# Performance work log

Measured on AMD Instinct MI355X. Metric: run time of the kernel, lower is better.

Reference implementation:

```python
import jax, jax.numpy as jnp
import numpy as np

B, H_IMG, W_IMG, K = 4, 60, 80, 8
HW = H_IMG * W_IMG
IMG_D, PT_D = 192, 128
NH, DH = 6, 64
INNER = NH * DH
NHF = 6
POS_D = 2 * (2 * NHF + 1)  # harmonic emb of 2-d offset, append_input=True -> 26
MAX_DIST = 0.1


def setup_inputs() -> dict:
    key = jax.random.key(0)
    ks = jax.random.split(key, 6)
    ys, xs = jnp.meshgrid(jnp.linspace(0.0, 1.0, H_IMG), jnp.linspace(0.0, 1.0, W_IMG), indexing='ij')
    img_uv = jnp.stack([xs.reshape(-1), ys.reshape(-1)], axis=-1)  # [HW, 2], normalized pixel grid
    return {
        'feat_2d': jax.random.normal(ks[0], (B, HW, IMG_D), jnp.float32),
        'feat_3d': jax.random.normal(ks[1], (B, HW, PT_D), jnp.float32),
        'proj_uv': jax.random.uniform(ks[2], (B, HW, 2), dtype=jnp.float32),
        'img_uv': img_uv,
        'ln_gamma': jnp.ones((IMG_D,), jnp.float32),
        'q_gamma': jnp.ones((NH, DH), jnp.float32),
        'k_gamma': jnp.ones((NH, DH), jnp.float32),
        'Wq': jax.random.normal(ks[3], (IMG_D, INNER), jnp.float32) * IMG_D ** -0.5,
        'Wkv': jax.random.normal(ks[4], (PT_D + POS_D, 2 * INNER), jnp.float32) * (PT_D + POS_D) ** -0.5,
        'Wout': jax.random.normal(ks[5], (INNER, INNER), jnp.float32) * INNER ** -0.5,
    }


def _layernorm(x, g, eps=1e-5):
    mu = jnp.mean(x, -1, keepdims=True)
    var = jnp.mean((x - mu) ** 2, -1, keepdims=True)
    return (x - mu) * jax.lax.rsqrt(var + eps) * g


def _rmsnorm(x, g):
    # lucidrains-style query/key RMSNorm: l2-normalize last dim, scale by sqrt(dim) * per-head gamma
    n = jnp.maximum(jnp.linalg.norm(x, axis=-1, keepdims=True), 1e-12)
    return x / n * (DH ** 0.5) * g


def reference(feat_2d, feat_3d, proj_uv, img_uv, ln_gamma, q_gamma, k_gamma, Wq, Wkv, Wout):
    # --- kNN: for each image pixel, k nearest projected points (brute force) ---
    d2 = (jnp.sum(img_uv ** 2, -1)[None, :, None]
          + jnp.sum(proj_uv ** 2, -1)[:, None, :]
          - 2.0 * jnp.einsum('qd,bnd->bqn', img_uv, proj_uv))  # [B, HW, HW]
    idx = jax.lax.top_k(-d2, K)[1]  # [B, HW, K] int32 indices

    # --- gather neighbor uv coords and 3d features ---
    knn_uv = img_uv[idx]                                        # [B, HW, K, 2]
    knn_f3 = jnp.take_along_axis(feat_3d, idx.reshape(B, HW * K, 1), axis=1).reshape(B, HW, K, PT_D)
    offset = knn_uv - img_uv[None, :, None, :]                  # [B, HW, K, 2]
    mask = jnp.sum(offset ** 2, -1) <= MAX_DIST ** 2            # [B, HW, K]

    # --- harmonic positional embedding of offsets ---
    freqs = 2.0 ** jnp.arange(NHF, dtype=jnp.float32)
    e = (offset[..., None] * freqs).reshape(B, HW, K, 2 * NHF)
    pos = jnp.concatenate([jnp.sin(e), jnp.cos(e), offset], -1)  # [B, HW, K, 26]

    # --- Q / K / V projections ---
    q = (_layernorm(feat_2d, ln_gamma) @ Wq).reshape(B, HW, NH, DH)
    kv = jnp.concatenate([knn_f3, pos], -1) @ Wkv               # [B, HW, K, 2*INNER]
    k_, v_ = jnp.split(kv, 2, axis=-1)
    k_ = k_.reshape(B, HW, K, NH, DH)
    v_ = v_.reshape(B, HW, K, NH, DH)
    q = _rmsnorm(q, q_gamma)
    k_ = _rmsnorm(k_, k_gamma)

    # --- tiny per-pixel attention (query len 1, key len K), scale=1.0 ---
    scores = jnp.einsum('bnhd,bnkhd->bnhk', q, k_)              # [B, HW, NH, K]
    scores = jnp.where(mask[:, :, None, :], scores, -1e30)
    attn = jax.nn.softmax(scores, axis=-1)
    out = jnp.einsum('bnhk,bnkhd->bnhd', attn, v_).reshape(B, HW, INNER)
    return out @ Wout  # output_type='1d': [B, HW, INNER]
```

## Files before the change

### kernel.cpp

```cpp
#include <hip/hip_runtime.h>
#include <math.h>

#define B_    4
#define HW_   4800
#define K_    8
#define IMGD  192
#define PTD   128
#define NH_   6
#define DH_   64
#define INNER 384
#define KVIN  154
#define QT    8
#define NJ    64
#define XBS   168
#define AST   392
#define KTQ   6
#define KTK   5
#define KTO   12

typedef _Float16 f16;
typedef __attribute__((ext_vector_type(8))) _Float16 f16x8;
typedef __attribute__((ext_vector_type(4))) float f32x4;

__global__ __launch_bounds__(256) void pack_kernel(
    const float* __restrict__ Wq, const float* __restrict__ Wkv,
    const float* __restrict__ Wout, f16* __restrict__ pw)
{
  const int e = blockIdx.x * 256 + threadIdx.x;
  if (e >= 672 * 512) return;
  const int f = e >> 9, r = e & 511, l = r >> 3, j = r & 7;
  const int lm = l & 15, kin = (l >> 4) * 8 + j;
  float v;
  if (f < 144) {
    const int nt = f / 6, kt = f % 6;
    v = Wq[(size_t)(kt * 32 + kin) * INNER + nt * 16 + lm];
  } else if (f < 264) {
    const int g = f - 144, nt = g / 5, kt = g % 5, k = kt * 32 + kin;
    v = (k < KVIN) ? Wkv[(size_t)k * (2 * INNER) + nt * 16 + lm] : 0.f;
  } else if (f < 384) {
    const int g = f - 264, nt = g / 5, kt = g % 5, k = kt * 32 + kin;
    v = (k < KVIN) ? Wkv[(size_t)k * (2 * INNER) + INNER + nt * 16 + lm] : 0.f;
  } else {
    const int g = f - 384, nt = g / 12, kt = g % 12;
    v = Wout[(size_t)(kt * 32 + kin) * INNER + nt * 16 + lm];
  }
  pw[e] = (f16)v;
}

#define KNN_INIT(d, ind)                                                      \
  _Pragma("unroll") for (int s = 0; s < K_; ++s) { d[s] = 3.4e38f; ind[s] = 0x7fffffff; }

#define KNN_INSERT(dd, n, dist, ind)                                          \
  if (dd < dist[K_ - 1]) {                                                    \
    bool placed = false;                                                      \
    _Pragma("unroll") for (int s = K_ - 1; s >= 1; --s) {                     \
      if (!placed) {                                                          \
        if (dd < dist[s - 1]) { dist[s] = dist[s - 1]; ind[s] = ind[s - 1]; } \
        else                  { dist[s] = dd; ind[s] = n; placed = true; }    \
      }                                                                       \
    }                                                                         \
    if (!placed) { dist[0] = dd; ind[0] = n; }                                \
  }

#define KNN_MERGE(dist, ind, qidx)                                            \
  _Pragma("unroll") for (int r = 0; r < K_; ++r) {                            \
    float hd = dist[0]; int hi = ind[0];                                      \
    float bd = hd; int bi = hi;                                               \
    _Pragma("unroll") for (int m = 1; m < 64; m <<= 1) {                      \
      float od = __shfl_xor(bd, m); int oi = __shfl_xor(bi, m);               \
      if (od < bd || (od == bd && oi < bi)) { bd = od; bi = oi; }             \
    }                                                                         \
    const bool won = (hd == bd && hi == bi);                                  \
    _Pragma("unroll") for (int s = 0; s < K_ - 1; ++s) {                      \
      dist[s] = won ? dist[s + 1] : dist[s];                                  \
      ind[s]  = won ? ind[s + 1]  : ind[s];                                   \
    }                                                                         \
    dist[K_ - 1] = won ? 3.4e38f : dist[K_ - 1];                              \
    ind[K_ - 1]  = won ? 0x7fffffff : ind[K_ - 1];                            \
    if (lane == r) idx_out[((size_t)b * HW_ + (qidx)) * K_ + r] = bi;         \
  }

__global__ __launch_bounds__(256) void knn_kernel(
    const float* __restrict__ proj_uv,
    const float* __restrict__ img_uv,
    int* __restrict__ idx_out)
{
#pragma clang fp contract(off)
  __shared__ float2 s_p[HW_];

  const int tid  = threadIdx.x;
  const int wave = tid >> 6;
  const int lane = tid & 63;
  const int blk  = blockIdx.x;
  const int b    = blk / (HW_ / 8);
  const int qA   = (blk % (HW_ / 8)) * 8 + wave * 2;
  const int qB   = qA + 1;

  const float2* pv = reinterpret_cast<const float2*>(proj_uv + (size_t)b * HW_ * 2);
  for (int i = tid; i < HW_; i += 256) s_p[i] = pv[i];
  __syncthreads();

  const float qxA = img_uv[qA * 2], qyA = img_uv[qA * 2 + 1];
  const float qxB = img_uv[qB * 2], qyB = img_uv[qB * 2 + 1];
  const float sqqA = qxA * qxA + qyA * qyA;
  const float sqqB = qxB * qxB + qyB * qyB;

  float dA[K_], dB[K_];
  int   iA[K_], iB[K_];
  KNN_INIT(dA, iA);
  KNN_INIT(dB, iB);

  for (int n = lane; n < HW_; n += 64) {
    const float2 p = s_p[n];
    const float sqp = p.x * p.x + p.y * p.y;
    const float dotA = fmaf(qyA, p.y, qxA * p.x);
    const float ddA  = (sqqA + sqp) - 2.0f * dotA;
    KNN_INSERT(ddA, n, dA, iA);
    const float dotB = fmaf(qyB, p.y, qxB * p.x);
    const float ddB  = (sqqB + sqp) - 2.0f * dotB;
    KNN_INSERT(ddB, n, dB, iB);
  }

  KNN_MERGE(dA, iA, qA);
  KNN_MERGE(dB, iB, qB);
}

__global__ __launch_bounds__(256, 4) void fused_kernel(
    const float* __restrict__ feat_2d,
    const float* __restrict__ feat_3d,
    const float* __restrict__ img_uv,
    const float* __restrict__ ln_gamma,
    const float* __restrict__ q_gamma,
    const float* __restrict__ k_gamma,
    const f16*   __restrict__ pw,
    const int*   __restrict__ idx_ws,
    float* __restrict__ out)
{
  __shared__ alignas(16) f16   s_X[NJ][XBS];
  __shared__ alignas(16) float s_regA[QT * AST];
  __shared__ float s_scores[NJ][NH_];
  __shared__ float s_attn[QT][NH_][K_];
  __shared__ float s_mask[NJ];
  __shared__ int   s_idx[NJ];
  __shared__ float s_offx[NJ];
  __shared__ float s_offy[NJ];
  __shared__ float s_norm[QT * NH_];

  f16* s_f16 = reinterpret_cast<f16*>(s_regA);

  const int tid = threadIdx.x;
  const int b   = blockIdx.y;
  const int q0  = blockIdx.x * QT;
  const int l   = tid & 63;
  const int w   = tid >> 6;
  const int lm  = l & 15;
  const int lg  = l >> 4;

  const f16* pwq = pw;
  const f16* pwk = pw + 144 * 512;
  const f16* pwv = pw + 264 * 512;
  const f16* pwo = pw + 384 * 512;

  if (tid < NJ) {
    const int j  = tid;
    const int q  = q0 + (j >> 3);
    const int id = idx_ws[((size_t)b * HW_ + q) * K_ + (j & 7)];
    s_idx[j] = id;
    const float ax = img_uv[id * 2], ay = img_uv[id * 2 + 1];
    const float bx = img_uv[q * 2],  by = img_uv[q * 2 + 1];
    s_offx[j] = ax - bx; s_offy[j] = ay - by;
    const double dox = (double)ax - (double)bx;
    const double doy = (double)ay - (double)by;
    s_mask[j] = (dox * dox + doy * doy <= 0.010000000000000002) ? 1.f : 0.f;
  }
  {
    unsigned* z = (unsigned*)(s_f16 + 8 * AST);
    for (int o = tid; o < 4 * AST; o += 256) z[o] = 0u;
  }
  {
    const int r  = ((tid >> 6) << 1) | ((tid >> 5) & 1);
    const int sl = tid & 31;
    const float* row = feat_2d + ((size_t)b * HW_ + q0 + r) * IMGD;
    float x[6]; float sum = 0.f, ssq = 0.f;
#pragma unroll
    for (int i = 0; i < 6; ++i) { x[i] = row[sl + 32 * i]; sum += x[i]; ssq += x[i] * x[i]; }
#pragma unroll
    for (int m = 16; m >= 1; m >>= 1) { sum += __shfl_xor(sum, m); ssq += __shfl_xor(ssq, m); }
    const float mu = sum * (1.f / 192.f);
    float var = ssq * (1.f / 192.f) - mu * mu;
    var = fmaxf(var, 0.f);
    const float rstd = rsqrtf(var + 1e-5f);
#pragma unroll
    for (int i = 0; i < 6; ++i) {
      const int c = sl + 32 * i;
      s_f16[r * AST + c] = (f16)((x[i] - mu) * rstd * ln_gamma[c]);
    }
  }
  __syncthreads();

  const int jX = tid >> 2, tsub = tid & 3;
  float4 xf[8];
  {
    const float4* f4 = reinterpret_cast<const float4*>(
        feat_3d + ((size_t)b * HW_ + s_idx[jX]) * PTD) + tsub * 8;
#pragma unroll
    for (int i = 0; i < 8; ++i) xf[i] = f4[i];
  }
  f32x4 qacc[6];
#pragma unroll
  for (int t = 0; t < 6; ++t) qacc[t] = (f32x4){0.f, 0.f, 0.f, 0.f};
  {
    const f16* ar = s_f16 + lm * AST + lg * 8;
#pragma unroll
    for (int kt = 0; kt < KTQ; ++kt) {
      const f16x8 a = *(const f16x8*)(ar + kt * 32);
#pragma unroll
      for (int t = 0; t < 6; ++t) {
        const int nt = w * 6 + t;
        const f16x8 bf = *(const f16x8*)(pwq + (((nt * 6 + kt) << 6) + l) * 8);
        qacc[t] = __builtin_amdgcn_mfma_f32_16x16x32_f16(a, bf, qacc[t], 0, 0, 0);
      }
    }
  }
  {
    f16* xr = &s_X[jX][tsub * 32];
#pragma unroll
    for (int i = 0; i < 8; ++i) {
      xr[i * 4 + 0] = (f16)xf[i].x; xr[i * 4 + 1] = (f16)xf[i].y;
      xr[i * 4 + 2] = (f16)xf[i].z; xr[i * 4 + 3] = (f16)xf[i].w;
    }
    if (tsub == 0) {
      const float ox = s_offx[jX], oy = s_offy[jX];
      f16* xp = &s_X[jX][PTD];
#pragma unroll
      for (int m = 0; m < 6; ++m) {
        const float fr = (float)(1 << m);
        float sx, cx, sy, cy;
        sincosf(ox * fr, &sx, &cx);
        sincosf(oy * fr, &sy, &cy);
        xp[m] = (f16)sx; xp[6 + m] = (f16)sy;
        xp[12 + m] = (f16)cx; xp[18 + m] = (f16)cy;
      }
      xp[24] = (f16)ox; xp[25] = (f16)oy;
#pragma unroll
      for (int m = 26; m < 32; ++m) xp[m] = (f16)0.f;
    }
  }
  __syncthreads();

  if (lg < 2) {
#pragma unroll
    for (int t = 0; t < 6; ++t) {
#pragma unroll
      for (int reg = 0; reg < 4; ++reg) {
        s_regA[(lg * 4 + reg) * AST + (w * 6 + t) * 16 + lm] = qacc[t][reg];
      }
    }
  }
  __syncthreads();

  if (tid < QT * NH_) {
    const int r = tid / NH_, h = tid % NH_;
    const float* v = s_regA + r * AST + h * DH_;
    float ss = 0.f;
#pragma unroll
    for (int d = 0; d < DH_; ++d) ss += v[d] * v[d];
    s_norm[tid] = fmaxf(sqrtf(ss), 1e-12f);
  }
  __syncthreads();

  {
    const int r  = tid >> 5;
    const int c0 = (tid & 31) * 12;
#pragma unroll
    for (int i = 0; i < 12; ++i) {
      const int c = c0 + i;
      const float n = s_norm[r * NH_ + (c >> 6)];
      s_regA[r * AST + c] *= (8.f / n) * q_gamma[c];
    }
  }
  __syncthreads();

  {
    const f16* xh = &s_X[16 * w + lm][lg * 8];
    f16x8 ax[KTK];
#pragma unroll
    for (int kt = 0; kt < KTK; ++kt) ax[kt] = *(const f16x8*)(xh + kt * 32);
    const int rq = 2 * w + (lg >> 1);
    for (int h = 0; h < NH_; ++h) {
      f32x4 kacc[4];
#pragma unroll
      for (int t = 0; t < 4; ++t) kacc[t] = (f32x4){0.f, 0.f, 0.f, 0.f};
#pragma unroll
      for (int kt = 0; kt < KTK; ++kt) {
#pragma unroll
        for (int t = 0; t < 4; ++t) {
          const int nt = h * 4 + t;
          const f16x8 bf = *(const f16x8*)(pwk + (((nt * 5 + kt) << 6) + l) * 8);
          kacc[t] = __builtin_amdgcn_mfma_f32_16x16x32_f16(ax[kt], bf, kacc[t], 0, 0, 0);
        }
      }
      float ss[4], sc[4];
#pragma unroll
      for (int reg = 0; reg < 4; ++reg) { ss[reg] = 0.f; sc[reg] = 0.f; }
#pragma unroll
      for (int t = 0; t < 4; ++t) {
        const int n = h * DH_ + t * 16 + lm;
        const float qg = s_regA[rq * AST + n] * k_gamma[n];
#pragma unroll
        for (int reg = 0; reg < 4; ++reg) {
          const float v = kacc[t][reg];
          ss[reg] += v * v;
          sc[reg] += v * qg;
        }
      }
#pragma unroll
      for (int m = 1; m < 16; m <<= 1) {
#pragma unroll
        for (int reg = 0; reg < 4; ++reg) {
          ss[reg] += __shfl_xor(ss[reg], m);
          sc[reg] += __shfl_xor(sc[reg], m);
        }
      }
      if (lm == 0) {
#pragma unroll
        for (int reg = 0; reg < 4; ++reg) {
          const float nn = fmaxf(sqrtf(ss[reg]), 1e-12f);
          s_scores[16 * w + (lg << 2) + reg][h] = (8.f / nn) * sc[reg];
        }
      }
    }
  }
  __syncthreads();

  if (tid < QT * NH_) {
    const int r = tid / NH_, h = tid % NH_;
    float s[K_]; float mx = -1e38f;
#pragma unroll
    for (int k = 0; k < K_; ++k) {
      float v = s_scores[r * K_ + k][h];
      if (s_mask[r * K_ + k] == 0.f) v = -1e30f;
      s[k] = v; mx = fmaxf(mx, v);
    }
    float sum = 0.f;
#pragma unroll
    for (int k = 0; k < K_; ++k) { const float pp = expf(s[k] - mx); s[k] = pp; sum += pp; }
    const float inv = 1.f / sum;
#pragma unroll
    for (int k = 0; k < K_; ++k) s_attn[r][h][k] = s[k] * inv;
  }
  __syncthreads();

  {
    unsigned* z = (unsigned*)(s_f16 + 8 * AST);
    for (int o = tid; o < 4 * AST; o += 256) z[o] = 0u;
  }
  {
    const int k0 = (lg & 1) * 4;
#pragma unroll
    for (int mt = 0; mt < 4; ++mt) {
      const f16* xh = &s_X[16 * mt + lm][lg * 8];
      f16x8 av[KTK];
#pragma unroll
      for (int kt = 0; kt < KTK; ++kt) av[kt] = *(const f16x8*)(xh + kt * 32);
      const int qrow = 2 * mt + (lg >> 1);
#pragma unroll
      for (int t = 0; t < 6; ++t) {
        const int nt = w * 6 + t;
        const int h  = nt >> 2;
        f32x4 c = (f32x4){0.f, 0.f, 0.f, 0.f};
#pragma unroll
        for (int kt = 0; kt < KTK; ++kt) {
          const f16x8 bf = *(const f16x8*)(pwv + (((nt * 5 + kt) << 6) + l) * 8);
          c = __builtin_amdgcn_mfma_f32_16x16x32_f16(av[kt], bf, c, 0, 0, 0);
        }
        const float4 at = *(const float4*)&s_attn[qrow][h][k0];
        float p = at.x * c[0] + at.y * c[1] + at.z * c[2] + at.w * c[3];
        p += __shfl_xor(p, 16);
        if ((lg & 1) == 0) s_f16[qrow * AST + nt * 16 + lm] = (f16)p;
      }
    }
  }
  __syncthreads();

  {
    f32x4 oacc[6];
#pragma unroll
    for (int t = 0; t < 6; ++t) oacc[t] = (f32x4){0.f, 0.f, 0.f, 0.f};
    const f16* ar = s_f16 + lm * AST + lg * 8;
#pragma unroll
    for (int kt = 0; kt < KTO; ++kt) {
      const f16x8 a = *(const f16x8*)(ar + kt * 32);
#pragma unroll
      for (int t = 0; t < 6; ++t) {
        const int nt = w * 6 + t;
        const f16x8 bf = *(const f16x8*)(pwo + (((nt * 12 + kt) << 6) + l) * 8);
        oacc[t] = __builtin_amdgcn_mfma_f32_16x16x32_f16(a, bf, oacc[t], 0, 0, 0);
      }
    }
    if (lg < 2) {
      float* orow0 = out + ((size_t)b * HW_ + q0) * INNER;
#pragma unroll
      for (int reg = 0; reg < 4; ++reg) {
        const int m = lg * 4 + reg;
#pragma unroll
        for (int t = 0; t < 6; ++t) {
          orow0[(size_t)m * INNER + (w * 6 + t) * 16 + lm] = oacc[t][reg];
        }
      }
    }
  }
}

extern "C" void kernel_launch(void* const* d_in, const int* in_sizes, int n_in,
                              void* d_out, int out_size, void* d_ws, size_t ws_size,
                              hipStream_t stream) {
  (void)in_sizes; (void)n_in; (void)out_size; (void)ws_size;
  const float* feat_2d = (const float*)d_in[0];
  const float* feat_3d = (const float*)d_in[1];
  const float* proj_uv = (const float*)d_in[2];
  const float* img_uv  = (const float*)d_in[3];
  const float* ln_g    = (const float*)d_in[4];
  const float* q_g     = (const float*)d_in[5];
  const float* k_g     = (const float*)d_in[6];
  const float* Wq      = (const float*)d_in[7];
  const float* Wkv     = (const float*)d_in[8];
  const float* Wout    = (const float*)d_in[9];
  float* out = (float*)d_out;

  int* idx_ws = (int*)d_ws;
  f16* pw = (f16*)((char*)d_ws + 614400);

  pack_kernel<<<dim3(1344), 256, 0, stream>>>(Wq, Wkv, Wout, pw);
  knn_kernel<<<dim3(B_ * HW_ / 8), 256, 0, stream>>>(proj_uv, img_uv, idx_ws);
  fused_kernel<<<dim3(HW_ / QT, B_), 256, 0, stream>>>(
      feat_2d, feat_3d, img_uv, ln_g, q_g, k_g, pw, idx_ws, out);
}
```

Measured before the change: 320.4 us.

## Process four queries per wave in kNN and restructure K/V MFMA loops for weight reuse

The kNN kernel now handles four queries per wave instead of two, halving the block count and reusing each shared-memory point load across more queries. In the fused kernel, the K projection is re-split so each wave owns one 16-column tile per head across all row tiles, keeping its weight fragments in registers. Per-row sum-of-squares and score partials are accumulated with shared-memory atomics, followed by an extra sync and a finalize pass. The V loop is reordered so weight fragments are loaded once per column tile, and block indices are remapped to spread neighbouring query tiles across blocks. The costs are more registers in kNN, extra LDS atomics, and an additional barrier.

```diff
diff --git a/kernel.cpp b/kernel.cpp
--- a/kernel.cpp
+++ b/kernel.cpp
@@ -92,37 +92,46 @@
   const int wave = tid >> 6;
   const int lane = tid & 63;
   const int blk  = blockIdx.x;
-  const int b    = blk / (HW_ / 8);
-  const int qA   = (blk % (HW_ / 8)) * 8 + wave * 2;
-  const int qB   = qA + 1;
+  const int b    = blk / (HW_ / 16);
+  const int q0   = (blk % (HW_ / 16)) * 16 + wave * 4;
 
   const float2* pv = reinterpret_cast<const float2*>(proj_uv + (size_t)b * HW_ * 2);
   for (int i = tid; i < HW_; i += 256) s_p[i] = pv[i];
   __syncthreads();
 
-  const float qxA = img_uv[qA * 2], qyA = img_uv[qA * 2 + 1];
-  const float qxB = img_uv[qB * 2], qyB = img_uv[qB * 2 + 1];
-  const float sqqA = qxA * qxA + qyA * qyA;
-  const float sqqB = qxB * qxB + qyB * qyB;
-
-  float dA[K_], dB[K_];
-  int   iA[K_], iB[K_];
-  KNN_INIT(dA, iA);
-  KNN_INIT(dB, iB);
+  float qx[4], qy[4], sqq[4];
+#pragma unroll
+  for (int c = 0; c < 4; ++c) {
+    qx[c] = img_uv[(q0 + c) * 2];
+    qy[c] = img_uv[(q0 + c) * 2 + 1];
+    sqq[c] = qx[c] * qx[c] + qy[c] * qy[c];
+  }
+
+  float dA[K_], dB[K_], dC[K_], dD[K_];
+  int   iA[K_], iB[K_], iC[K_], iD[K_];
+  KNN_INIT(dA, iA); KNN_INIT(dB, iB); KNN_INIT(dC, iC); KNN_INIT(dD, iD);
 
   for (int n = lane; n < HW_; n += 64) {
     const float2 p = s_p[n];
     const float sqp = p.x * p.x + p.y * p.y;
-    const float dotA = fmaf(qyA, p.y, qxA * p.x);
-    const float ddA  = (sqqA + sqp) - 2.0f * dotA;
-    KNN_INSERT(ddA, n, dA, iA);
-    const float dotB = fmaf(qyB, p.y, qxB * p.x);
-    const float ddB  = (sqqB + sqp) - 2.0f * dotB;
-    KNN_INSERT(ddB, n, dB, iB);
-  }
-
-  KNN_MERGE(dA, iA, qA);
-  KNN_MERGE(dB, iB, qB);
+    const float t0 = fmaf(qy[0], p.y, qx[0] * p.x);
+    const float e0 = (sqq[0] + sqp) - 2.0f * t0;
+    KNN_INSERT(e0, n, dA, iA);
+    const float t1 = fmaf(qy[1], p.y, qx[1] * p.x);
+    const float e1 = (sqq[1] + sqp) - 2.0f * t1;
+    KNN_INSERT(e1, n, dB, iB);
+    const float t2 = fmaf(qy[2], p.y, qx[2] * p.x);
+    const float e2 = (sqq[2] + sqp) - 2.0f * t2;
+    KNN_INSERT(e2, n, dC, iC);
+    const float t3 = fmaf(qy[3], p.y, qx[3] * p.x);
+    const float e3 = (sqq[3] + sqp) - 2.0f * t3;
+    KNN_INSERT(e3, n, dD, iD);
+  }
+
+  KNN_MERGE(dA, iA, q0 + 0);
+  KNN_MERGE(dB, iB, q0 + 1);
+  KNN_MERGE(dC, iC, q0 + 2);
+  KNN_MERGE(dD, iD, q0 + 3);
 }
 
 __global__ __launch_bounds__(256, 4) void fused_kernel(
@@ -139,7 +148,8 @@
   __shared__ alignas(16) f16   s_X[NJ][XBS];
   __shared__ alignas(16) float s_regA[QT * AST];
   __shared__ float s_scores[NJ][NH_];
-  __shared__ float s_attn[QT][NH_][K_];
+  __shared__ float s_kss[NJ][NH_];
+  __shared__ float s_ksc[NJ][NH_];
   __shared__ float s_mask[NJ];
   __shared__ int   s_idx[NJ];
   __shared__ float s_offx[NJ];
@@ -147,10 +157,12 @@
   __shared__ float s_norm[QT * NH_];
 
   f16* s_f16 = reinterpret_cast<f16*>(s_regA);
+  float (*s_attn)[NH_][K_] = reinterpret_cast<float (*)[NH_][K_]>(&s_kss[0][0]);
 
   const int tid = threadIdx.x;
   const int b   = blockIdx.y;
-  const int q0  = blockIdx.x * QT;
+  const int bx  = (blockIdx.x & 7) * 75 + (blockIdx.x >> 3);
+  const int q0  = bx * QT;
   const int l   = tid & 63;
   const int w   = tid >> 6;
   const int lm  = l & 15;
@@ -167,10 +179,10 @@
     const int id = idx_ws[((size_t)b * HW_ + q) * K_ + (j & 7)];
     s_idx[j] = id;
     const float ax = img_uv[id * 2], ay = img_uv[id * 2 + 1];
-    const float bx = img_uv[q * 2],  by = img_uv[q * 2 + 1];
-    s_offx[j] = ax - bx; s_offy[j] = ay - by;
-    const double dox = (double)ax - (double)bx;
-    const double doy = (double)ay - (double)by;
+    const float bx2 = img_uv[q * 2], by2 = img_uv[q * 2 + 1];
+    s_offx[j] = ax - bx2; s_offy[j] = ay - by2;
+    const double dox = (double)ax - (double)bx2;
+    const double doy = (double)ay - (double)by2;
     s_mask[j] = (dox * dox + doy * doy <= 0.010000000000000002) ? 1.f : 0.f;
   }
   {
@@ -279,57 +291,61 @@
       s_regA[r * AST + c] *= (8.f / n) * q_gamma[c];
     }
   }
-  __syncthreads();
-
-  {
-    const f16* xh = &s_X[16 * w + lm][lg * 8];
-    f16x8 ax[KTK];
-#pragma unroll
-    for (int kt = 0; kt < KTK; ++kt) ax[kt] = *(const f16x8*)(xh + kt * 32);
-    const int rq = 2 * w + (lg >> 1);
+  for (int o = tid; o < NJ * NH_; o += 256) {
+    s_kss[o / NH_][o % NH_] = 0.f;
+    s_ksc[o / NH_][o % NH_] = 0.f;
+  }
+  __syncthreads();
+
+  {
     for (int h = 0; h < NH_; ++h) {
-      f32x4 kacc[4];
-#pragma unroll
-      for (int t = 0; t < 4; ++t) kacc[t] = (f32x4){0.f, 0.f, 0.f, 0.f};
-#pragma unroll
-      for (int kt = 0; kt < KTK; ++kt) {
-#pragma unroll
-        for (int t = 0; t < 4; ++t) {
-          const int nt = h * 4 + t;
-          const f16x8 bf = *(const f16x8*)(pwk + (((nt * 5 + kt) << 6) + l) * 8);
-          kacc[t] = __builtin_amdgcn_mfma_f32_16x16x32_f16(ax[kt], bf, kacc[t], 0, 0, 0);
+      const int nt  = h * 4 + w;
+      const int col = nt * 16 + lm;
+      f16x8 bf[KTK];
+#pragma unroll
+      for (int kt = 0; kt < KTK; ++kt)
+        bf[kt] = *(const f16x8*)(pwk + (((nt * KTK + kt) << 6) + l) * 8);
+      const float kg = k_gamma[col];
+#pragma unroll
+      for (int mt = 0; mt < 4; ++mt) {
+        const f16* xh = &s_X[16 * mt + lm][lg * 8];
+        f32x4 c = (f32x4){0.f, 0.f, 0.f, 0.f};
+#pragma unroll
+        for (int kt = 0; kt < KTK; ++kt)
+          c = __builtin_amdgcn_mfma_f32_16x16x32_f16(
+              *(const f16x8*)(xh + kt * 32), bf[kt], c, 0, 0, 0);
+        const int rq = 2 * mt + (lg >> 1);
+        const float qg = s_regA[rq * AST + col] * kg;
+        float ss[4], sc[4];
+#pragma unroll
+        for (int reg = 0; reg < 4; ++reg) {
+          const float v = c[reg];
+          ss[reg] = v * v; sc[reg] = v * qg;
         }
-      }
-      float ss[4], sc[4];
-#pragma unroll
-      for (int reg = 0; reg < 4; ++reg) { ss[reg] = 0.f; sc[reg] = 0.f; }
-#pragma unroll
-      for (int t = 0; t < 4; ++t) {
-        const int n = h * DH_ + t * 16 + lm;
-        const float qg = s_regA[rq * AST + n] * k_gamma[n];
-#pragma unroll
-        for (int reg = 0; reg < 4; ++reg) {
-          const float v = kacc[t][reg];
-          ss[reg] += v * v;
-          sc[reg] += v * qg;
+#pragma unroll
+        for (int m = 1; m < 16; m <<= 1) {
+#pragma unroll
+          for (int reg = 0; reg < 4; ++reg) {
+            ss[reg] += __shfl_xor(ss[reg], m);
+            sc[reg] += __shfl_xor(sc[reg], m);
+          }
         }
-      }
-#pragma unroll
-      for (int m = 1; m < 16; m <<= 1) {
-#pragma unroll
-        for (int reg = 0; reg < 4; ++reg) {
-          ss[reg] += __shfl_xor(ss[reg], m);
-          sc[reg] += __shfl_xor(sc[reg], m);
+        if (lm == 0) {
+#pragma unroll
+          for (int reg = 0; reg < 4; ++reg) {
+            const int row = 16 * mt + 4 * lg + reg;
+            atomicAdd(&s_kss[row][h], ss[reg]);
+            atomicAdd(&s_ksc[row][h], sc[reg]);
+          }
         }
       }
-      if (lm == 0) {
-#pragma unroll
-        for (int reg = 0; reg < 4; ++reg) {
-          const float nn = fmaxf(sqrtf(ss[reg]), 1e-12f);
-          s_scores[16 * w + (lg << 2) + reg][h] = (8.f / nn) * sc[reg];
-        }
-      }
-    }
+    }
+  }
+  __syncthreads();
+  for (int o = tid; o < NJ * NH_; o += 256) {
+    const int row = o / NH_, h = o - row * NH_;
+    const float nn = fmaxf(sqrtf(s_kss[row][h]), 1e-12f);
+    s_scores[row][h] = (8.f / nn) * s_ksc[row][h];
   }
   __syncthreads();
 
@@ -358,22 +374,22 @@
   {
     const int k0 = (lg & 1) * 4;
 #pragma unroll
-    for (int mt = 0; mt < 4; ++mt) {
-      const f16* xh = &s_X[16 * mt + lm][lg * 8];
-      f16x8 av[KTK];
-#pragma unroll
-      for (int kt = 0; kt < KTK; ++kt) av[kt] = *(const f16x8*)(xh + kt * 32);
-      const int qrow = 2 * mt + (lg >> 1);
-#pragma unroll
-      for (int t = 0; t < 6; ++t) {
-        const int nt = w * 6 + t;
-        const int h  = nt >> 2;
+    for (int t = 0; t < 6; ++t) {
+      const int nt = w * 6 + t;
+      const int h  = nt >> 2;
+      f16x8 bf[KTK];
+#pragma unroll
+      for (int kt = 0; kt < KTK; ++kt)
+        bf[kt] = *(const f16x8*)(pwv + (((nt * KTK + kt) << 6) + l) * 8);
+#pragma unroll
+      for (int mt = 0; mt < 4; ++mt) {
+        const f16* xh = &s_X[16 * mt + lm][lg * 8];
         f32x4 c = (f32x4){0.f, 0.f, 0.f, 0.f};
 #pragma unroll
-        for (int kt = 0; kt < KTK; ++kt) {
-          const f16x8 bf = *(const f16x8*)(pwv + (((nt * 5 + kt) << 6) + l) * 8);
-          c = __builtin_amdgcn_mfma_f32_16x16x32_f16(av[kt], bf, c, 0, 0, 0);
-        }
+        for (int kt = 0; kt < KTK; ++kt)
+          c = __builtin_amdgcn_mfma_f32_16x16x32_f16(
+              *(const f16x8*)(xh + kt * 32), bf[kt], c, 0, 0, 0);
+        const int qrow = 2 * mt + (lg >> 1);
         const float4 at = *(const float4*)&s_attn[qrow][h][k0];
         float p = at.x * c[0] + at.y * c[1] + at.z * c[2] + at.w * c[3];
         p += __shfl_xor(p, 16);
@@ -432,7 +448,7 @@
   f16* pw = (f16*)((char*)d_ws + 614400);
 
   pack_kernel<<<dim3(1344), 256, 0, stream>>>(Wq, Wkv, Wout, pw);
-  knn_kernel<<<dim3(B_ * HW_ / 8), 256, 0, stream>>>(proj_uv, img_uv, idx_ws);
+  knn_kernel<<<dim3(B_ * HW_ / 16), 256, 0, stream>>>(proj_uv, img_uv, idx_ws);
   fused_kernel<<<dim3(HW_ / QT, B_), 256, 0, stream>>>(
       feat_2d, feat_3d, img_uv, ln_g, q_g, k_g, pw, idx_ws, out);
 }
```

Result: no change. 316.2 us (-1.3%).
